# Performance work log

Measured on AMD Instinct MI355X. Metric: run time of the kernel, lower is better.

Reference implementation:

```python
import jax, jax.numpy as jnp
import numpy as np

D = 128
H = 8
B = 4
L = 2048


def setup_inputs() -> dict:
    key = jax.random.key(0)
    ks = jax.random.split(key, 5)
    s = 1.0 / np.sqrt(D)
    x = jax.random.normal(ks[0], (B, L, D), dtype=jnp.float32)
    Wq = jax.random.normal(ks[1], (D, D * H), dtype=jnp.float32) * s
    Wk = jax.random.normal(ks[2], (D, D * H), dtype=jnp.float32) * s
    Wv = jax.random.normal(ks[3], (D, D * H), dtype=jnp.float32) * s
    Wu = jax.random.normal(ks[4], (D * H, D), dtype=jnp.float32) * (1.0 / np.sqrt(D * H))
    bu = jnp.zeros((D,), dtype=jnp.float32)
    return {"x": x, "Wq": Wq, "Wk": Wk, "Wv": Wv, "Wu": Wu, "bu": bu}


def reference(x, Wq, Wk, Wv, Wu, bu):
    b, l, d = x.shape
    h = H
    # project and split heads: [b, l, h, d] -> [b, h, l, d]
    q = (x @ Wq).reshape(b, l, h, d).transpose(0, 2, 1, 3)
    k = (x @ Wk).reshape(b, l, h, d).transpose(0, 2, 1, 3)
    v = (x @ Wv).reshape(b, l, h, d).transpose(0, 2, 1, 3)
    scores = jnp.einsum("bhqd,bhkd->bhqk", q, k) / jnp.sqrt(jnp.float32(d))
    w = jax.nn.softmax(scores, axis=-1)
    out = jnp.einsum("bhqk,bhkd->bhqd", w, v)  # [b, h, l, d]
    out = out.transpose(0, 2, 1, 3).reshape(b, l, h * d)
    return out @ Wu + bu
```

## Files before the change

### kernel.cpp

```cpp
#include <hip/hip_runtime.h>
#include <stdint.h>

#define D_ 128
#define H_ 8
#define B_ 4
#define L_ 2048
#define NH (B_*H_)

typedef __bf16 bf16x8 __attribute__((ext_vector_type(8)));
typedef float f32x4 __attribute__((ext_vector_type(4)));
typedef float f32x16 __attribute__((ext_vector_type(16)));
typedef unsigned short u16;
typedef u16 u16x2 __attribute__((ext_vector_type(2)));
typedef u16 u16x4 __attribute__((ext_vector_type(4)));
typedef u16 u16x8 __attribute__((ext_vector_type(8)));
typedef uint32_t u32x2 __attribute__((ext_vector_type(2)));
typedef uint32_t u32x4 __attribute__((ext_vector_type(4)));
typedef float fvec4 __attribute__((ext_vector_type(4)));

__device__ __forceinline__ u16 f2b(float f){
    uint32_t u = __builtin_bit_cast(uint32_t, f);
    u += 0x7fffu + ((u >> 16) & 1u);
    return (u16)(u >> 16);
}
__device__ __forceinline__ u16 f2b_native(float f){
    return __builtin_bit_cast(u16, (__bf16)f);
}
__device__ __forceinline__ uint32_t pk2(float a, float b){
    u16x2 v = { f2b_native(a), f2b_native(b) };
    return __builtin_bit_cast(uint32_t, v);
}
__device__ __forceinline__ float ex2(float x){
#if __has_builtin(__builtin_amdgcn_exp2f)
    return __builtin_amdgcn_exp2f(x);
#else
    return exp2f(x);
#endif
}
__device__ __forceinline__ u32x2 permswap(uint32_t a, uint32_t b){
#if __has_builtin(__builtin_amdgcn_permlane32_swap)
    return __builtin_amdgcn_permlane32_swap(a, b, false, false);
#else
    asm volatile("v_permlane32_swap_b32 %0, %1" : "+v"(a), "+v"(b));
    u32x2 r; r[0] = a; r[1] = b; return r;
#endif
}
__device__ __forceinline__ bf16x8 asbf(u16x8 v){ return __builtin_bit_cast(bf16x8, v); }
#define MFMA(a,b,c)   __builtin_amdgcn_mfma_f32_16x16x32_bf16((a),(b),(c),0,0,0)
#define MFMA32(a,b,c) __builtin_amdgcn_mfma_f32_32x32x16_bf16((a),(b),(c),0,0,0)

__device__ __forceinline__ void gld16(const u16* g, u16* l){
    __builtin_amdgcn_global_load_lds(
        (const __attribute__((address_space(1))) void*)g,
        (__attribute__((address_space(3))) void*)l, 16, 0, 0);
}

__global__ __launch_bounds__(256)
void cvt_all(const float* __restrict__ x, const float* __restrict__ Wq,
             const float* __restrict__ Wk, const float* __restrict__ Wv,
             const float* __restrict__ Wu,
             u16* __restrict__ xb, u16* __restrict__ wT, u16* __restrict__ wuT)
{
    const int blk = blockIdx.x;
    const int t = threadIdx.x;
    if (blk < 512){
        size_t i = ((size_t)blk*256 + t)*8;
        fvec4 lo = *(const fvec4*)&x[i];
        fvec4 hi = *(const fvec4*)&x[i+4];
        u16x8 u;
        for (int j=0;j<4;++j){ u[j]=f2b(lo[j]); u[4+j]=f2b(hi[j]); }
        *(u16x8*)&xb[i] = u;
        return;
    }
    __shared__ __align__(16) u16 T[128][144];
    const int b = blk - 512;
    const float* src; int ld, coff, roff; u16* dst;
    if (b < 24){
        int mat = b>>3, head = b&7;
        src = (mat==0)?Wq:((mat==1)?Wk:Wv); ld = D_*H_; coff = head*128; roff = 0;
        dst = wT + (size_t)b*16384;
    } else {
        src = Wu; ld = D_; coff = 0; roff = (b-24)*128;
        dst = wuT + (size_t)(b-24)*16384;
    }
    for (int it=0; it<16; ++it){
        int k = it*8 + (t>>5), n0 = (t&31)*4;
        fvec4 wv = *(const fvec4*)&src[(size_t)(roff+k)*ld + coff + n0];
        for (int i=0;i<4;++i) T[n0+i][k] = f2b(wv[i]);
    }
    __syncthreads();
    for (int it=0; it<8; ++it){
        int gi = it*256 + t; int n = gi>>4, g = gi&15;
        *(u16x8*)&dst[n*128 + g*8] = *(const u16x8*)&T[n][(g^(n&7))*8];
    }
}

__global__ __launch_bounds__(256)
void qkv_proj(const u16* __restrict__ xb, const u16* __restrict__ wT,
              u16* __restrict__ q_ws, u16* __restrict__ k_ws, u16* __restrict__ v_ws)
{
    const int head = blockIdx.x;
    const int rt   = blockIdx.y;
    const int mat  = blockIdx.z;

    __shared__ __align__(16) u16 Xs[128*128];
    __shared__ __align__(16) u16 Ws[128*128];

    const int t = threadIdx.x;
    const int row0 = rt*128;
    const u16* wsrc = wT + (size_t)(mat*8 + head)*16384;

    for (int it=0; it<8; ++it){
        int gi = it*256 + t;
        int r = gi>>4, g = gi&15;
        gld16(&xb[(size_t)(row0+r)*D_ + ((g ^ (r&7))*8)], &Xs[(it*256 + (t>>6)*64)*8]);
        gld16(&wsrc[gi*8],                                &Ws[(it*256 + (t>>6)*64)*8]);
    }
    asm volatile("s_waitcnt vmcnt(0)" ::: "memory");
    __builtin_amdgcn_s_barrier();

    const int wave = t>>6, lane = t&63;
    const int wr = wave>>1, wc = wave&1;
    const int lrow = lane&15, lgrp = lane>>4;
    const int swz = lrow&7;

    f32x4 acc[4][4] = {};
    #pragma unroll
    for (int kc=0;kc<4;++kc){
        const int gd = kc*4 + lgrp;
        bf16x8 a[4], bfr[4];
        #pragma unroll
        for (int mr=0;mr<4;++mr)
            a[mr] = asbf(*(const u16x8*)&Xs[(wr*64+mr*16+lrow)*128 + ((gd ^ swz)*8)]);
        #pragma unroll
        for (int nr=0;nr<4;++nr)
            bfr[nr] = asbf(*(const u16x8*)&Ws[(wc*64+nr*16+lrow)*128 + ((gd ^ swz)*8)]);
        #pragma unroll
        for (int mr=0;mr<4;++mr)
            #pragma unroll
            for (int nr=0;nr<4;++nr)
                acc[mr][nr] = MFMA(a[mr], bfr[nr], acc[mr][nr]);
    }

    const float qscale = 0.12751879455370425f;
    for (int mr=0;mr<4;++mr){
        for (int nr=0;nr<4;++nr){
            f32x4 v = acc[mr][nr];
            int baserow = row0 + wr*64 + mr*16 + lgrp*4;
            int cd = wc*64 + nr*16 + lrow;
            int b  = baserow / L_;
            int l  = baserow % L_;
            int bh = b*H_ + head;
            if (mat==2){
                u16x4 pv;
                for (int r=0;r<4;++r) pv[r] = f2b(v[r]);
                *(u16x4*)&v_ws[((size_t)bh*D_ + cd)*L_ + l] = pv;
            } else {
                u16* dst = (mat==0) ? q_ws : k_ws;
                for (int r=0;r<4;++r){
                    float f = v[r];
                    if (mat==0) f *= qscale;
                    dst[((size_t)bh*L_ + (l + r))*D_ + cd] = f2b(f);
                }
            }
        }
    }
}

__global__ __launch_bounds__(512)
void attn(const u16* __restrict__ q_ws, const u16* __restrict__ k_ws,
          const u16* __restrict__ v_ws, u16* __restrict__ o_ws)
{
    const int wg = ((blockIdx.x & 7) << 5) | (blockIdx.x >> 3);
    const int qt = wg & 7;
    const int bh = wg >> 3;

    const int t = threadIdx.x, wave = t>>6, lane = t&63;
    const int q31 = lane & 31;
    const int hi  = lane >> 5;
    const int swq = q31 & 7;

    __shared__ __align__(16) u16 Kb[4][64*128];
    __shared__ __align__(16) u16 Vb[4][128*64];

    const int q0 = qt*256 + wave*32;

    bf16x8 qf[8];
    #pragma unroll
    for (int ks=0; ks<8; ++ks)
        qf[ks] = asbf(*(const u16x8*)&q_ws[((size_t)bh*L_ + q0 + q31)*D_ + ks*16 + hi*8]);

    const u16* kp = k_ws + (size_t)bh*L_*D_;
    const u16* vp = v_ws + (size_t)bh*D_*L_;
    int koff[2], voff[2];
    #pragma unroll
    for (int i=0;i<2;++i){
        int f = i*512 + t;
        int kr = f>>4, kc = f&15;
        koff[i] = kr*128 + ((kc ^ (kr&7))*8);
        int vr = f>>3, vc = f&7;
        voff[i] = vr*L_ + ((vc ^ (vr&7))*8);
    }

    auto stage = [&](int buf){
        #pragma unroll
        for (int i=0;i<2;++i){
            gld16(kp + koff[i], &Kb[buf][(i*512 + wave*64)*8]);
            gld16(vp + voff[i], &Vb[buf][(i*512 + wave*64)*8]);
        }
        kp += 64*D_;
        vp += 64;
    };

    auto qkt = [&](int buf, f32x16& S0, f32x16& S1){
        f32x16 s0a = {}, s0b = {}, s1a = {}, s1b = {};
        #pragma unroll
        for (int ks=0; ks<4; ++ks){
            bf16x8 ka0 = asbf(*(const u16x8*)&Kb[buf][q31*128      + (((ks*2+hi)     ^ swq)*8)]);
            bf16x8 ka1 = asbf(*(const u16x8*)&Kb[buf][q31*128      + ((((ks+4)*2+hi) ^ swq)*8)]);
            bf16x8 kb0 = asbf(*(const u16x8*)&Kb[buf][(32+q31)*128 + (((ks*2+hi)     ^ swq)*8)]);
            bf16x8 kb1 = asbf(*(const u16x8*)&Kb[buf][(32+q31)*128 + ((((ks+4)*2+hi) ^ swq)*8)]);
            s0a = MFMA32(ka0, qf[ks],   s0a);
            s0b = MFMA32(ka1, qf[ks+4], s0b);
            s1a = MFMA32(kb0, qf[ks],   s1a);
            s1b = MFMA32(kb1, qf[ks+4], s1b);
        }
        S0 = s0a + s0b;
        S1 = s1a + s1b;
    };

    float lsA = 0.f, lsB = 0.f;
    f32x16 o4[4] = {};

    stage(0);
    stage(1);
    stage(2);
    asm volatile("s_waitcnt vmcnt(4)" ::: "memory");
    __builtin_amdgcn_s_barrier();

    f32x16 sP0, sP1, sN0, sN1;
    qkt(0, sP0, sP1);

    const int NT = L_/64;
    for (int kt=0; kt<NT; ++kt){
        const int cur = kt & 3;
        if (kt < NT-3) stage((kt+3) & 3);

        __builtin_amdgcn_s_setprio(1);
        if (kt < NT-1) qkt((kt+1) & 3, sN0, sN1);
        __builtin_amdgcn_s_setprio(0);

        #define SM_PV(SREG, KS) do { \
            float p0 = ex2(SREG[((KS&1)*8)+0]); \
            float p1 = ex2(SREG[((KS&1)*8)+1]); \
            float p2 = ex2(SREG[((KS&1)*8)+2]); \
            float p3 = ex2(SREG[((KS&1)*8)+3]); \
            float p4 = ex2(SREG[((KS&1)*8)+4]); \
            float p5 = ex2(SREG[((KS&1)*8)+5]); \
            float p6 = ex2(SREG[((KS&1)*8)+6]); \
            float p7 = ex2(SREG[((KS&1)*8)+7]); \
            lsA += (p0+p1)+(p2+p3); \
            lsB += (p4+p5)+(p6+p7); \
            uint32_t cA = pk2(p0,p1), cB = pk2(p2,p3); \
            uint32_t cC = pk2(p4,p5), cD = pk2(p6,p7); \
            u32x2 r0 = permswap(cA, cC); \
            u32x2 r1 = permswap(cB, cD); \
            u32x4 wv; \
            wv[0] = r0[0];  wv[1] = r1[0]; \
            wv[2] = r0[1];  wv[3] = r1[1]; \
            bf16x8 pa = __builtin_bit_cast(bf16x8, wv); \
            __builtin_amdgcn_s_setprio(1); \
            _Pragma("unroll") \
            for (int nc2=0; nc2<4; ++nc2){ \
                bf16x8 vb = asbf(*(const u16x8*)&Vb[cur][ (nc2*32+q31)*64 + (((KS*2+hi) ^ swq)*8) ]); \
                o4[nc2] = MFMA32(pa, vb, o4[nc2]); \
            } \
            __builtin_amdgcn_s_setprio(0); \
        } while(0)

        SM_PV(sP0, 0);
        SM_PV(sP0, 1);
        SM_PV(sP1, 2);
        SM_PV(sP1, 3);
        #undef SM_PV

        if (kt < NT-1){
            if (kt <= NT-4) asm volatile("s_waitcnt vmcnt(4)" ::: "memory");
            else            asm volatile("s_waitcnt vmcnt(0)" ::: "memory");
            __builtin_amdgcn_s_barrier();
        }
        sP0 = sN0;
        sP1 = sN1;
    }

    float lsum = lsA + lsB;
    lsum += __shfl_xor(lsum, 32, 64);
    float inv = 1.0f / lsum;

    const int b = bh / H_, h = bh % H_;
    #pragma unroll
    for (int m=0; m<4; ++m){
        #pragma unroll
        for (int i=0; i<4; ++i){
            const int reg = m*4 + i;
            const int row = i + 8*m + 4*hi;
            float riv = __shfl(inv, row, 64);
            const int l = q0 + row;
            size_t base = ((size_t)(b*L_ + l))*(D_*H_) + h*128 + q31;
            #pragma unroll
            for (int nc2=0; nc2<4; ++nc2)
                o_ws[base + nc2*32] = f2b_native(o4[nc2][reg] * riv);
        }
    }
}

__global__ __launch_bounds__(256)
void out_proj(const u16* __restrict__ o_ws, const u16* __restrict__ wuT,
              const float* __restrict__ bu, float* __restrict__ out)
{
    const int rt = blockIdx.x;
    const int t = threadIdx.x, wave = t>>6, lane = t&63;
    const int wr = wave>>1, wc = wave&1;
    const int lrow = lane&15, lgrp = lane>>4;
    const int swz = lrow&7;

    __shared__ __align__(16) u16 As[2][32*128];
    __shared__ __align__(16) u16 Ws[2][128*128];

    const int row0 = rt*32;
    f32x4 acc[4] = {};

    auto stage = [&](int ks){
        const int buf = ks & 1;
        int gi = t;
        int r = gi>>4, g = gi&15;
        gld16(&o_ws[(size_t)(row0+r)*(D_*H_) + ks*128 + ((g ^ (r&7))*8)], &As[buf][((t>>6)*64)*8]);
        gi = 256 + t;
        r = gi>>4; g = gi&15;
        gld16(&o_ws[(size_t)(row0+r)*(D_*H_) + ks*128 + ((g ^ (r&7))*8)], &As[buf][(256 + (t>>6)*64)*8]);
        const u16* wsrc = wuT + (size_t)ks*16384;
        #pragma unroll
        for (int it=0; it<8; ++it)
            gld16(&wsrc[(it*256 + t)*8], &Ws[buf][(it*256 + (t>>6)*64)*8]);
    };

    stage(0);
    for (int ks=0; ks<8; ++ks){
        const int buf = ks & 1;
        if (ks < 7){
            stage(ks+1);
            asm volatile("s_waitcnt vmcnt(10)" ::: "memory");
        } else {
            asm volatile("s_waitcnt vmcnt(0)" ::: "memory");
        }
        __builtin_amdgcn_s_barrier();

        #pragma unroll
        for (int kc=0;kc<4;++kc){
            const int gd = kc*4 + lgrp;
            bf16x8 a = asbf(*(const u16x8*)&As[buf][(wr*16+lrow)*128 + ((gd ^ swz)*8)]);
            #pragma unroll
            for (int nc=0;nc<4;++nc){
                bf16x8 b = asbf(*(const u16x8*)&Ws[buf][(wc*64+nc*16+lrow)*128 + ((gd ^ swz)*8)]);
                acc[nc] = MFMA(a, b, acc[nc]);
            }
        }
        __builtin_amdgcn_s_barrier();
    }

    for (int nc=0;nc<4;++nc){
        for (int r=0;r<4;++r){
            int row = row0 + wr*16 + lgrp*4 + r;
            int n = wc*64 + nc*16 + lrow;
            out[(size_t)row*D_ + n] = acc[nc][r] + bu[n];
        }
    }
}

extern "C" void kernel_launch(void* const* d_in, const int* in_sizes, int n_in,
                              void* d_out, int out_size, void* d_ws, size_t ws_size,
                              hipStream_t stream)
{
    const float* x  = (const float*)d_in[0];
    const float* Wq = (const float*)d_in[1];
    const float* Wk = (const float*)d_in[2];
    const float* Wv = (const float*)d_in[3];
    const float* Wu = (const float*)d_in[4];
    const float* bu = (const float*)d_in[5];
    float* out = (float*)d_out;

    u16* ws = (u16*)d_ws;
    const size_t SZ = (size_t)NH * L_ * D_;
    u16* q_ws = ws;
    u16* k_ws = q_ws + SZ;
    u16* v_ws = k_ws + SZ;
    u16* o_ws = v_ws + SZ;
    u16* x_bf = o_ws + SZ;
    u16* wT   = x_bf + (size_t)B_*L_*D_;
    u16* wuT  = wT + 24*16384;

    cvt_all<<<dim3(544), 256, 0, stream>>>(x, Wq, Wk, Wv, Wu, x_bf, wT, wuT);
    qkv_proj<<<dim3(H_, (B_*L_)/128, 3), 256, 0, stream>>>(x_bf, wT, q_ws, k_ws, v_ws);
    attn<<<dim3((L_/256)*NH), 512, 0, stream>>>(q_ws, k_ws, v_ws, o_ws);
    out_proj<<<dim3((B_*L_)/32), 256, 0, stream>>>(o_ws, wuT, bu, out);
}
```

Before: 119.3 us.

## Pre-tile K and V workspaces so attention tiles load contiguously into LDS

The projection kernel now writes K and V into a blocked layout: 64-row tiles, with 8-element column groups laid out contiguously. The attention kernel can then stage each tile with plain linear 16-byte global loads and no per-thread swizzled offsets. The LDS reads use the group-major layout instead of XOR swizzling, which removes the address arithmetic and makes the global reads fully coalesced. The K stores in the projection become scattered 2-byte writes, and LDS bank-conflict behaviour changes, which may help or hurt.

Measured after the change: 120.5 us. No clear change (+1.0%).

```diff
diff --git a/kernel.cpp b/kernel.cpp
--- a/kernel.cpp
+++ b/kernel.cpp
@@ -154,14 +154,17 @@
             if (mat==2){
                 u16x4 pv;
                 for (int r=0;r<4;++r) pv[r] = f2b(v[r]);
-                *(u16x4*)&v_ws[((size_t)bh*D_ + cd)*L_ + l] = pv;
+                size_t va = (size_t)bh*D_*L_ + (size_t)(l>>6)*8192 + ((l&63)>>3)*1024 + cd*8 + (l&7);
+                *(u16x4*)&v_ws[va] = pv;
+            } else if (mat==1){
+                for (int r=0;r<4;++r){
+                    int l2 = l + r;
+                    size_t ka = (size_t)bh*L_*D_ + (size_t)(l2>>6)*8192 + (cd>>3)*512 + (l2&63)*8 + (cd&7);
+                    k_ws[ka] = f2b(v[r]);
+                }
             } else {
-                u16* dst = (mat==0) ? q_ws : k_ws;
-                for (int r=0;r<4;++r){
-                    float f = v[r];
-                    if (mat==0) f *= qscale;
-                    dst[((size_t)bh*L_ + (l + r))*D_ + cd] = f2b(f);
-                }
+                for (int r=0;r<4;++r)
+                    q_ws[((size_t)bh*L_ + (l + r))*D_ + cd] = f2b(v[r]*qscale);
             }
         }
     }
@@ -178,7 +181,6 @@
     const int t = threadIdx.x, wave = t>>6, lane = t&63;
     const int q31 = lane & 31;
     const int hi  = lane >> 5;
-    const int swq = q31 & 7;
 
     __shared__ __align__(16) u16 Kb[4][64*128];
     __shared__ __align__(16) u16 Vb[4][128*64];
@@ -192,34 +194,26 @@
 
     const u16* kp = k_ws + (size_t)bh*L_*D_;
     const u16* vp = v_ws + (size_t)bh*D_*L_;
-    int koff[2], voff[2];
-    #pragma unroll
-    for (int i=0;i<2;++i){
-        int f = i*512 + t;
-        int kr = f>>4, kc = f&15;
-        koff[i] = kr*128 + ((kc ^ (kr&7))*8);
-        int vr = f>>3, vc = f&7;
-        voff[i] = vr*L_ + ((vc ^ (vr&7))*8);
-    }
 
     auto stage = [&](int buf){
         #pragma unroll
         for (int i=0;i<2;++i){
-            gld16(kp + koff[i], &Kb[buf][(i*512 + wave*64)*8]);
-            gld16(vp + voff[i], &Vb[buf][(i*512 + wave*64)*8]);
-        }
-        kp += 64*D_;
-        vp += 64;
+            gld16(kp + (i*512 + t)*8, &Kb[buf][(i*512 + wave*64)*8]);
+            gld16(vp + (i*512 + t)*8, &Vb[buf][(i*512 + wave*64)*8]);
+        }
+        kp += 8192;
+        vp += 8192;
     };
 
     auto qkt = [&](int buf, f32x16& S0, f32x16& S1){
         f32x16 s0a = {}, s0b = {}, s1a = {}, s1b = {};
         #pragma unroll
         for (int ks=0; ks<4; ++ks){
-            bf16x8 ka0 = asbf(*(const u16x8*)&Kb[buf][q31*128      + (((ks*2+hi)     ^ swq)*8)]);
-            bf16x8 ka1 = asbf(*(const u16x8*)&Kb[buf][q31*128      + ((((ks+4)*2+hi) ^ swq)*8)]);
-            bf16x8 kb0 = asbf(*(const u16x8*)&Kb[buf][(32+q31)*128 + (((ks*2+hi)     ^ swq)*8)]);
-            bf16x8 kb1 = asbf(*(const u16x8*)&Kb[buf][(32+q31)*128 + ((((ks+4)*2+hi) ^ swq)*8)]);
+            const int g0 = ks*2+hi, g1 = (ks+4)*2+hi;
+            bf16x8 ka0 = asbf(*(const u16x8*)&Kb[buf][g0*512 + q31*8]);
+            bf16x8 ka1 = asbf(*(const u16x8*)&Kb[buf][g1*512 + q31*8]);
+            bf16x8 kb0 = asbf(*(const u16x8*)&Kb[buf][g0*512 + (32+q31)*8]);
+            bf16x8 kb1 = asbf(*(const u16x8*)&Kb[buf][g1*512 + (32+q31)*8]);
             s0a = MFMA32(ka0, qf[ks],   s0a);
             s0b = MFMA32(ka1, qf[ks+4], s0b);
             s1a = MFMA32(kb0, qf[ks],   s1a);
@@ -272,7 +266,7 @@
             __builtin_amdgcn_s_setprio(1); \
             _Pragma("unroll") \
             for (int nc2=0; nc2<4; ++nc2){ \
-                bf16x8 vb = asbf(*(const u16x8*)&Vb[cur][ (nc2*32+q31)*64 + (((KS*2+hi) ^ swq)*8) ]); \
+                bf16x8 vb = asbf(*(const u16x8*)&Vb[cur][ (KS*2+hi)*1024 + (nc2*32+q31)*8 ]); \
                 o4[nc2] = MFMA32(pa, vb, o4[nc2]); \
             } \
             __builtin_amdgcn_s_setprio(0); \
```
